# Performance work log

Hardware: AMD Instinct MI355X
Metric: run time of the kernel (lower is better)

## Reference

```python
import jax, jax.numpy as jnp
import numpy as np

N = 100000      # nodes
E = 400000      # edges per relation
R = 4           # relations
D_IN, D_HID, D_OUT = 256, 256, 128


def setup_inputs() -> dict:
    key = jax.random.key(0)
    ks = jax.random.split(key, 6)
    x = jax.random.normal(ks[0], (N, D_IN), jnp.float32)
    src = jax.random.randint(ks[1], (R, E), 0, N)
    dst = jax.random.randint(ks[2], (R, E), 0, N)
    # glorot-ish init for per-relation GraphConv weights
    W1 = jax.random.normal(ks[3], (R, D_IN, D_HID), jnp.float32) * (1.0 / np.sqrt(D_IN))
    b1 = jnp.zeros((R, D_HID), jnp.float32)
    W2 = jax.random.normal(ks[4], (R, D_HID, D_OUT), jnp.float32) * (1.0 / np.sqrt(D_HID))
    b2 = jnp.zeros((R, D_OUT), jnp.float32)
    return {"x": x, "src": src, "dst": dst, "W1": W1, "b1": b1, "W2": W2, "b2": b2}


def _rel_graphconv(x, src, dst, W, b):
    """DGL GraphConv with norm='both': D_dst^{-1/2} A D_src^{-1/2} X W + b.
    x: [N, din]; src/dst: [E]; W: [din, dout]; b: [dout]."""
    n = x.shape[0]
    xw = x @ W                                                   # [N, dout]
    ones = jnp.ones(src.shape, jnp.float32)
    out_deg = jnp.maximum(jax.ops.segment_sum(ones, src, num_segments=n), 1.0)
    in_deg = jnp.maximum(jax.ops.segment_sum(ones, dst, num_segments=n), 1.0)
    msg = xw[src] * (out_deg[src] ** -0.5)[:, None]              # [E, dout] gather + src-norm
    agg = jax.ops.segment_sum(msg, dst, num_segments=n)          # [N, dout] scatter-add
    return agg * (in_deg ** -0.5)[:, None] + b


def _hetero_layer(x, src, dst, W, b):
    # HeteroGraphConv(aggregate='sum'): run GraphConv per relation, sum results.
    conv = jax.vmap(_rel_graphconv, in_axes=(None, 0, 0, 0, 0))
    return jnp.sum(conv(x, src, dst, W, b), axis=0)              # [N, dout]


def reference(x, src, dst, W1, b1, W2, b2):
    h = jax.nn.relu(_hetero_layer(x, src, dst, W1, b1))
    return _hetero_layer(h, src, dst, W2, b2)
```

## Files before the change

### kernel.cpp

```cpp
#include <hip/hip_runtime.h>


#define RELS 4
#define DIN 256
#define DHID 256
#define DOUT 128

typedef short short8 __attribute__((ext_vector_type(8)));
typedef unsigned short ushort8 __attribute__((ext_vector_type(8)));
typedef float f32x4 __attribute__((ext_vector_type(4)));


__device__ __forceinline__ unsigned short f2bf(float f) {
    unsigned int u = __float_as_uint(f);
    u += 0x7FFFu + ((u >> 16) & 1u);
    return (unsigned short)(u >> 16);
}
__device__ __forceinline__ float bf2f(unsigned short u) {
    return __uint_as_float(((unsigned int)u) << 16);
}


__global__ void hist_kernel(const int* __restrict__ src, const int* __restrict__ dst,
                            int* __restrict__ cnt_src, int* __restrict__ cnt_dst,
                            int* __restrict__ rank, int E, int N) {
    int i = blockIdx.x * blockDim.x + threadIdx.x;
    if (i >= RELS * E) return;
    int r = i / E;
    atomicAdd(cnt_src + (size_t)r * N + src[i], 1);
    int rk = atomicAdd(cnt_dst + (size_t)r * N + dst[i], 1);
    rank[i] = rk;
}

__global__ void scan_norm(const int* __restrict__ counts, int* __restrict__ out,
                          int* __restrict__ blk_sums, int n, int SB,
                          const int* __restrict__ cnt, float* __restrict__ nrm, long nnorm) {
    if ((int)blockIdx.x < SB) {
        __shared__ int sh[256];
        int i = blockIdx.x * 256 + threadIdx.x;
        int v = (i < n) ? counts[i] : 0;
        sh[threadIdx.x] = v;
        __syncthreads();
#pragma unroll
        for (int off = 1; off < 256; off <<= 1) {
            int t = (threadIdx.x >= off) ? sh[threadIdx.x - off] : 0;
            __syncthreads();
            sh[threadIdx.x] += t;
            __syncthreads();
        }
        if (i < n) out[i] = sh[threadIdx.x] - v;
        if (threadIdx.x == 255) blk_sums[blockIdx.x] = sh[255];
    } else {
        long i = (long)(blockIdx.x - SB) * 256 + threadIdx.x;
        if (i < nnorm) nrm[i] = rsqrtf(fmaxf((float)cnt[i], 1.0f));
    }
}

__global__ void scan_sums(int* __restrict__ bs, int nb) {
    __shared__ int sh[256];
    __shared__ int carry;
    if (threadIdx.x == 0) carry = 0;
    __syncthreads();
    for (int base = 0; base < nb; base += 256) {
        int i = base + threadIdx.x;
        int v = (i < nb) ? bs[i] : 0;
        sh[threadIdx.x] = v;
        __syncthreads();
#pragma unroll
        for (int off = 1; off < 256; off <<= 1) {
            int t = (threadIdx.x >= off) ? sh[threadIdx.x - off] : 0;
            __syncthreads();
            sh[threadIdx.x] += t;
            __syncthreads();
        }
        if (i < nb) bs[i] = sh[threadIdx.x] - v + carry;
        int tot = sh[255];
        __syncthreads();
        if (threadIdx.x == 255) carry += tot;
        __syncthreads();
    }
}

__global__ void scan_add(int* __restrict__ out, const int* __restrict__ blk_sums,
                         int n, int total) {
    int i = blockIdx.x * 256 + threadIdx.x;
    if (i < n) out[i] += blk_sums[blockIdx.x];
    if (i == n - 1) out[n] = total;
}

__global__ void fill_kernel(const int* __restrict__ src, const int* __restrict__ dst,
                            const float* __restrict__ nsrc, const int* __restrict__ row_ptr,
                            const int* __restrict__ rank, int2* __restrict__ e_pack,
                            int E, int N) {
    int i = blockIdx.x * blockDim.x + threadIdx.x;
    if (i >= RELS * E) return;
    int r = i / E;
    int s = src[i];
    int pos = row_ptr[(size_t)r * N + dst[i]] + rank[i];
    e_pack[pos] = make_int2(s, __float_as_int(nsrc[(size_t)r * N + s]));
}


__global__ void prep_fused(const float* __restrict__ x, const float* __restrict__ W1,
                           const float* __restrict__ W2, const float* __restrict__ b1,
                           const float* __restrict__ b2,
                           unsigned short* __restrict__ x_bf, unsigned short* __restrict__ w1t,
                           unsigned short* __restrict__ w2t,
                           float* __restrict__ b1s, float* __restrict__ b2s, long n8x) {
    const int T1 = RELS * DIN * DHID;
    const int T2 = RELS * DHID * DOUT;
    long i = blockIdx.x * (long)blockDim.x + threadIdx.x;
    if (i < n8x) {
        const float4* ip = (const float4*)(x + i * 8);
        float4 v0 = ip[0], v1 = ip[1];
        ushort4 o0 = make_ushort4(f2bf(v0.x), f2bf(v0.y), f2bf(v0.z), f2bf(v0.w));
        ushort4 o1 = make_ushort4(f2bf(v1.x), f2bf(v1.y), f2bf(v1.z), f2bf(v1.w));
        ushort4* op = (ushort4*)(x_bf + i * 8);
        op[0] = o0; op[1] = o1;
    } else if (i < n8x + T1) {
        int j = (int)(i - n8x);
        int r = j / (DIN * DHID);
        int rem = j - r * (DIN * DHID);
        int k = rem / DHID, n = rem - k * DHID;
        w1t[(size_t)n * (RELS * DIN) + r * DIN + k] = f2bf(W1[j]);
    } else if (i < n8x + T1 + T2) {
        int j = (int)(i - n8x - T1);
        int r = j / (DHID * DOUT);
        int rem = j - r * (DHID * DOUT);
        int k = rem / DOUT, n = rem - k * DOUT;
        w2t[((size_t)r * DOUT + n) * DHID + k] = f2bf(W2[j]);
    } else if (i < n8x + T1 + T2 + DHID + DOUT) {
        int c = (int)(i - n8x - T1 - T2);
        if (c < DHID) {
            b1s[c] = b1[c] + b1[DHID + c] + b1[2 * DHID + c] + b1[3 * DHID + c];
        } else {
            int cc = c - DHID;
            b2s[cc] = b2[cc] + b2[DOUT + cc] + b2[2 * DOUT + cc] + b2[3 * DOUT + cc];
        }
    }
}


__device__ __forceinline__ void gload_lds16(const void* g, void* l) {
    __builtin_amdgcn_global_load_lds(
        (const __attribute__((address_space(1))) void*)g,
        (__attribute__((address_space(3))) void*)l, 16, 0, 0);
}

template <int MODE>
__global__ __launch_bounds__(256) void gemm_bf16(
    const unsigned short* __restrict__ A, const unsigned short* __restrict__ Bt,
    unsigned short* __restrict__ C, int M, int Nout, int K,
    const float* __restrict__ scale_or_bias, int cols_per_rel, int Nnodes) {
    __shared__ unsigned short smA[128 * 32];
    __shared__ unsigned short smB[128 * 32];
    const int tid = threadIdx.x;
    const int lane = tid & 63;
    const int wid = tid >> 6;
    const int wr = wid >> 1, wc = wid & 1;
    const int brow = blockIdx.x * 128, bcol = blockIdx.y * 128;

    f32x4 acc[4][4] = {};

    const int s = lane >> 4;
    const int rl = lane & 15;

    for (int k0 = 0; k0 < K; k0 += 32) {
#pragma unroll
        for (int q = 0; q < 2; ++q) {
            int c = q * 256 + tid;
            int cl = c ^ ((c >> 3) & 3);
            int row = cl >> 2, slot = cl & 3;
            int ga = brow + row; ga = ga < M ? ga : M - 1;
            size_t ldsoff = (size_t)(q * 256 + (tid & ~63)) * 16;
            gload_lds16(A + (size_t)ga * K + k0 + slot * 8, (char*)smA + ldsoff);
            gload_lds16(Bt + (size_t)(bcol + row) * K + k0 + slot * 8, (char*)smB + ldsoff);
        }
        asm volatile("s_waitcnt vmcnt(0)" ::: "memory");
        __syncthreads();

        short8 a[4], b[4];
#pragma unroll
        for (int i = 0; i < 4; ++i) {
            int r = wr * 64 + i * 16 + rl;
            int ch = r * 4 + (s ^ ((r >> 1) & 3));
            a[i] = *(const short8*)((const char*)smA + ch * 16);
        }
#pragma unroll
        for (int j = 0; j < 4; ++j) {
            int r = wc * 64 + j * 16 + rl;
            int ch = r * 4 + (s ^ ((r >> 1) & 3));
            b[j] = *(const short8*)((const char*)smB + ch * 16);
        }
#pragma unroll
        for (int i = 0; i < 4; ++i)
#pragma unroll
            for (int j = 0; j < 4; ++j)
                acc[i][j] = __builtin_amdgcn_mfma_f32_16x16x32_bf16(a[i], b[j], acc[i][j], 0, 0, 0);
        __syncthreads();
    }

    const int rq = lane >> 4;
    if (MODE == 0) {
        const int relid = bcol / cols_per_rel;
        const float* nsr = scale_or_bias + (size_t)relid * Nnodes;
#pragma unroll
        for (int i = 0; i < 4; ++i) {
            int rbase = brow + wr * 64 + i * 16 + rq * 4;
            float sc[4];
#pragma unroll
            for (int t = 0; t < 4; ++t) {
                int row = rbase + t;
                sc[t] = (row < M) ? nsr[row] : 0.f;
            }
#pragma unroll
            for (int j = 0; j < 4; ++j) {
                int col = bcol + wc * 64 + j * 16 + rl;
#pragma unroll
                for (int t = 0; t < 4; ++t) {
                    int row = rbase + t;
                    if (row < M) C[(size_t)row * Nout + col] = f2bf(acc[i][j][t] * sc[t]);
                }
            }
        }
    } else {
#pragma unroll
        for (int i = 0; i < 4; ++i) {
            int rbase = brow + wr * 64 + i * 16 + rq * 4;
#pragma unroll
            for (int j = 0; j < 4; ++j) {
                int col = bcol + wc * 64 + j * 16 + rl;
                float bb = scale_or_bias[col];
#pragma unroll
                for (int t = 0; t < 4; ++t) {
                    int row = rbase + t;
                    if (row < M) C[(size_t)row * Nout + col] = f2bf(fmaxf(acc[i][j][t] + bb, 0.f));
                }
            }
        }
    }
}


__global__ void gather1_agg(const unsigned short* __restrict__ x_bf,
                            const int* __restrict__ rp, const int2* __restrict__ e_pack,
                            const float* __restrict__ ndst,
                            unsigned short* __restrict__ agg4, int N) {
    long w = (blockIdx.x * (long)blockDim.x + threadIdx.x) >> 6;
    int d = (int)(w >> 2);
    if (d >= N) return;
    int r = (int)(w & 3);
    int lane = threadIdx.x & 63;
    int h = lane >> 5, l = lane & 31;
    int beg = rp[(size_t)r * N + d], end = rp[(size_t)r * N + d + 1];
    float acc0[8] = {}, acc1[8] = {};
    int e = beg + h;
    for (; e + 2 < end; e += 4) {
        int2 p0 = e_pack[e];
        int2 p1 = e_pack[e + 2];
        ushort8 v0 = *(const ushort8*)(x_bf + (size_t)p0.x * DIN + l * 8);
        ushort8 v1 = *(const ushort8*)(x_bf + (size_t)p1.x * DIN + l * 8);
        float ns0 = __int_as_float(p0.y);
        float ns1 = __int_as_float(p1.y);
#pragma unroll
        for (int j = 0; j < 8; ++j) {
            acc0[j] += ns0 * bf2f(v0[j]);
            acc1[j] += ns1 * bf2f(v1[j]);
        }
    }
    if (e < end) {
        int2 p0 = e_pack[e];
        ushort8 v0 = *(const ushort8*)(x_bf + (size_t)p0.x * DIN + l * 8);
        float ns0 = __int_as_float(p0.y);
#pragma unroll
        for (int j = 0; j < 8; ++j) acc0[j] += ns0 * bf2f(v0[j]);
    }
    float nd = ndst[(size_t)r * N + d];
    ushort8 o;
#pragma unroll
    for (int j = 0; j < 8; ++j) {
        float v = acc0[j] + acc1[j];
        v += __shfl_xor(v, 32);
        o[j] = f2bf(nd * v);
    }
    if (h == 0)
        __builtin_nontemporal_store(o, (ushort8*)(agg4 + (size_t)d * (RELS * DIN) + r * DIN + l * 8));
}

__global__ void gather2_fused(const unsigned short* __restrict__ hw4,
                              const int* __restrict__ rp, const int2* __restrict__ e_pack,
                              const float* __restrict__ ndst, const float* __restrict__ b2s,
                              float* __restrict__ out, int N) {
    int wid = (int)((blockIdx.x * (long)blockDim.x + threadIdx.x) >> 6);
    if (wid >= N) return;
    int lane = threadIdx.x & 63;
    int h = lane >> 5, l = lane & 31;
    float oacc[4] = {};
#pragma unroll
    for (int r = 0; r < RELS; ++r) {
        int beg = rp[(size_t)r * N + wid], end = rp[(size_t)r * N + wid + 1];
        float acc0[4] = {}, acc1[4] = {};
        int e = beg + h;
        for (; e + 2 < end; e += 4) {
            int s0 = e_pack[e].x;
            int s1 = e_pack[e + 2].x;
            ushort4 v0 = *(const ushort4*)(hw4 + (size_t)s0 * (RELS * DOUT) + r * DOUT + l * 4);
            ushort4 v1 = *(const ushort4*)(hw4 + (size_t)s1 * (RELS * DOUT) + r * DOUT + l * 4);
            acc0[0] += bf2f(v0.x); acc0[1] += bf2f(v0.y); acc0[2] += bf2f(v0.z); acc0[3] += bf2f(v0.w);
            acc1[0] += bf2f(v1.x); acc1[1] += bf2f(v1.y); acc1[2] += bf2f(v1.z); acc1[3] += bf2f(v1.w);
        }
        if (e < end) {
            int s0 = e_pack[e].x;
            ushort4 v0 = *(const ushort4*)(hw4 + (size_t)s0 * (RELS * DOUT) + r * DOUT + l * 4);
            acc0[0] += bf2f(v0.x); acc0[1] += bf2f(v0.y); acc0[2] += bf2f(v0.z); acc0[3] += bf2f(v0.w);
        }
        float nd = ndst[(size_t)r * N + wid];
#pragma unroll
        for (int j = 0; j < 4; ++j) oacc[j] += nd * (acc0[j] + acc1[j]);
    }
#pragma unroll
    for (int j = 0; j < 4; ++j) oacc[j] += __shfl_xor(oacc[j], 32);
    if (h == 0) {
        f32x4 o;
        o[0] = oacc[0] + b2s[l * 4 + 0];
        o[1] = oacc[1] + b2s[l * 4 + 1];
        o[2] = oacc[2] + b2s[l * 4 + 2];
        o[3] = oacc[3] + b2s[l * 4 + 3];
        __builtin_nontemporal_store(o, (f32x4*)(out + (size_t)wid * DOUT + l * 4));
    }
}


extern "C" void kernel_launch(void* const* d_in, const int* in_sizes, int n_in,
                              void* d_out, int out_size, void* d_ws, size_t ws_size,
                              hipStream_t stream) {
    const float* x   = (const float*)d_in[0];
    const int*   src = (const int*)d_in[1];
    const int*   dst = (const int*)d_in[2];
    const float* W1  = (const float*)d_in[3];
    const float* b1  = (const float*)d_in[4];
    const float* W2  = (const float*)d_in[5];
    const float* b2  = (const float*)d_in[6];
    float* out = (float*)d_out;

    const int N = in_sizes[0] / DIN;
    const int E = in_sizes[1] / RELS;
    const int RN = RELS * N;

    char* p = (char*)d_ws;
    int*   cnt_src = (int*)p;    p += (size_t)RN * sizeof(int);
    int*   cnt_dst = (int*)p;    p += (size_t)RN * sizeof(int);
    float* nsrc    = (float*)p;  p += (size_t)RN * sizeof(float);
    float* ndst    = (float*)p;  p += (size_t)RN * sizeof(float);
    int*   row_ptr = (int*)p;    p += ((size_t)RN + 16) * sizeof(int);
    int*   rank    = (int*)p;    p += (size_t)RELS * E * sizeof(int);
    int2*  e_pack  = (int2*)p;   p += (size_t)RELS * E * sizeof(int2);
    int*   blk_sums= (int*)p;    p += 2048 * sizeof(int);
    float* b1s     = (float*)p;  p += DHID * sizeof(float);
    float* b2s     = (float*)p;  p += DOUT * sizeof(float);
    unsigned short* x_bf = (unsigned short*)p; p += (size_t)N * DIN * sizeof(short);
    unsigned short* w1t  = (unsigned short*)p; p += (size_t)RELS * DIN * DHID * sizeof(short);
    unsigned short* w2t  = (unsigned short*)p; p += (size_t)RELS * DHID * DOUT * sizeof(short);
    unsigned short* h_bf = (unsigned short*)p; p += (size_t)N * DHID * sizeof(short);
    unsigned short* agg4 = (unsigned short*)p; p += (size_t)N * RELS * DIN * sizeof(short);
    unsigned short* hw4  = agg4;

    const long n8x = (long)N * DIN / 8;
    {
        long tot = n8x + RELS * DIN * DHID + RELS * DHID * DOUT + DHID + DOUT;
        prep_fused<<<(int)((tot + 255) / 256), 256, 0, stream>>>(
            x, W1, W2, b1, b2, x_bf, w1t, w2t, b1s, b2s, n8x);
    }

    hipMemsetAsync(cnt_src, 0, (size_t)2 * RN * sizeof(int), stream);
    {
        int total = RELS * E;
        hist_kernel<<<(total + 255) / 256, 256, 0, stream>>>(
            src, dst, cnt_src, cnt_dst, rank, E, N);
    }

    const int nscan = (RN + 255) / 256;
    {
        long nnorm = (long)2 * RN;
        int NB = (int)((nnorm + 255) / 256);
        scan_norm<<<nscan + NB, 256, 0, stream>>>(
            cnt_dst, row_ptr, blk_sums, RN, nscan, cnt_src, nsrc, nnorm);
    }
    scan_sums<<<1, 256, 0, stream>>>(blk_sums, nscan);
    scan_add<<<nscan, 256, 0, stream>>>(row_ptr, blk_sums, RN, RELS * E);

    {
        int total = RELS * E;
        fill_kernel<<<(total + 255) / 256, 256, 0, stream>>>(
            src, dst, nsrc, row_ptr, rank, e_pack, E, N);
    }

    const int gx = (N + 127) / 128;

    {
        long waves = (long)RELS * N;
        int blocks = (int)((waves + 3) / 4);
        gather1_agg<<<blocks, 256, 0, stream>>>(x_bf, row_ptr, e_pack, ndst, agg4, N);
        dim3 grid(gx, DHID / 128);
        gemm_bf16<1><<<grid, 256, 0, stream>>>(agg4, w1t, h_bf, N, DHID, RELS * DIN, b1s, 0, N);
    }

    {
        dim3 grid(gx, (RELS * DOUT) / 128);
        gemm_bf16<0><<<grid, 256, 0, stream>>>(h_bf, w2t, hw4, N, RELS * DOUT, DHID, nsrc, DOUT, N);
        int gblocks = (N + 3) / 4;
        gather2_fused<<<gblocks, 256, 0, stream>>>(hw4, row_ptr, e_pack, ndst, b2s, out, N);
    }
}
```

Before: 738.3 us.

## Fuse layer-1 neighbor aggregation with the relation GEMM in one kernel

Replaces the separate gather1_agg kernel and the MODE 1 GEMM with one fused1 kernel. Each 512-thread block aggregates 128 destination rows per relation into LDS, then runs MFMA against that relation's weight slice, accumulating over all four relations before applying bias and ReLU. This removes the write and re-read of the N x 1024 bf16 agg4 intermediate in global memory. In exchange, B operands are loaded straight from global without LDS staging, there is one block per 128 rows (about 782 blocks), and the gather and GEMM phases are serialized by barriers, so occupancy and latency hiding drop.

```diff
diff --git a/kernel.cpp b/kernel.cpp
--- a/kernel.cpp
+++ b/kernel.cpp
@@ -141,17 +141,121 @@
 }
 
 
+#define LDP 264
+
+__global__ __launch_bounds__(512) void fused1(
+    const unsigned short* __restrict__ x_bf, const int* __restrict__ rp,
+    const int2* __restrict__ e_pack, const float* __restrict__ ndst,
+    const unsigned short* __restrict__ w1t, const float* __restrict__ b1s,
+    unsigned short* __restrict__ h_bf, int N) {
+    __shared__ __align__(16) unsigned short smA[128 * LDP];
+    const int tid = threadIdx.x;
+    const int lane = tid & 63;
+    const int wid = tid >> 6;
+    const int wr = wid >> 2, wc = wid & 3;
+    const int brow = blockIdx.x * 128;
+    const int s = lane >> 4, rl = lane & 15;
+    const int h = lane >> 5, l = lane & 31;
+
+    f32x4 acc[4][4] = {};
+
+    for (int r = 0; r < RELS; ++r) {
+#pragma unroll 2
+        for (int t = 0; t < 16; ++t) {
+            int row = wid * 16 + t;
+            int node = brow + row;
+            int beg = 0, end = 0;
+            float nd = 0.f;
+            if (node < N) {
+                int base = r * N + node;
+                beg = rp[base]; end = rp[base + 1];
+                nd = ndst[base];
+            }
+            float acc0[8] = {}, acc1[8] = {};
+            int e = beg + h;
+            for (; e + 2 < end; e += 4) {
+                int2 p0 = e_pack[e];
+                int2 p1 = e_pack[e + 2];
+                ushort8 v0 = *(const ushort8*)(x_bf + (size_t)p0.x * DIN + l * 8);
+                ushort8 v1 = *(const ushort8*)(x_bf + (size_t)p1.x * DIN + l * 8);
+                float ns0 = __int_as_float(p0.y);
+                float ns1 = __int_as_float(p1.y);
+#pragma unroll
+                for (int j = 0; j < 8; ++j) {
+                    acc0[j] += ns0 * bf2f(v0[j]);
+                    acc1[j] += ns1 * bf2f(v1[j]);
+                }
+            }
+            if (e < end) {
+                int2 p0 = e_pack[e];
+                ushort8 v0 = *(const ushort8*)(x_bf + (size_t)p0.x * DIN + l * 8);
+                float ns0 = __int_as_float(p0.y);
+#pragma unroll
+                for (int j = 0; j < 8; ++j) acc0[j] += ns0 * bf2f(v0[j]);
+            }
+            ushort8 o;
+#pragma unroll
+            for (int j = 0; j < 8; ++j) {
+                float v = acc0[j] + acc1[j];
+                v += __shfl_xor(v, 32);
+                o[j] = f2bf(nd * v);
+            }
+            if (h == 0)
+                *(ushort8*)(smA + (size_t)row * LDP + l * 8) = o;
+        }
+        __syncthreads();
+
+        const unsigned short* wb = w1t + (size_t)r * DIN;
+#pragma unroll 2
+        for (int k0 = 0; k0 < 256; k0 += 32) {
+            short8 a[4], b[4];
+#pragma unroll
+            for (int i = 0; i < 4; ++i) {
+                int arow = wr * 64 + i * 16 + rl;
+                a[i] = *(const short8*)(smA + (size_t)arow * LDP + k0 + s * 8);
+            }
+#pragma unroll
+            for (int j = 0; j < 4; ++j) {
+                int col = wc * 64 + j * 16 + rl;
+                b[j] = *(const short8*)(wb + (size_t)col * (RELS * DIN) + k0 + s * 8);
+            }
+#pragma unroll
+            for (int i = 0; i < 4; ++i)
+#pragma unroll
+                for (int j = 0; j < 4; ++j)
+                    acc[i][j] = __builtin_amdgcn_mfma_f32_16x16x32_bf16(a[i], b[j], acc[i][j], 0, 0, 0);
+        }
+        __syncthreads();
+    }
+
+    const int rq = lane >> 4;
+#pragma unroll
+    for (int i = 0; i < 4; ++i) {
+        int rbase = brow + wr * 64 + i * 16 + rq * 4;
+#pragma unroll
+        for (int j = 0; j < 4; ++j) {
+            int col = wc * 64 + j * 16 + rl;
+            float bb = b1s[col];
+#pragma unroll
+            for (int t = 0; t < 4; ++t) {
+                int row = rbase + t;
+                if (row < N) h_bf[(size_t)row * DHID + col] = f2bf(fmaxf(acc[i][j][t] + bb, 0.f));
+            }
+        }
+    }
+}
+
+
 __device__ __forceinline__ void gload_lds16(const void* g, void* l) {
     __builtin_amdgcn_global_load_lds(
         (const __attribute__((address_space(1))) void*)g,
         (__attribute__((address_space(3))) void*)l, 16, 0, 0);
 }
 
-template <int MODE>
 __global__ __launch_bounds__(256) void gemm_bf16(
     const unsigned short* __restrict__ A, const unsigned short* __restrict__ Bt,
     unsigned short* __restrict__ C, int M, int Nout, int K,
-    const float* __restrict__ scale_or_bias, int cols_per_rel, int Nnodes) {
+    const float* __restrict__ nsrc_all, int cols_per_rel, int Nnodes) {
     __shared__ unsigned short smA[128 * 32];
     __shared__ unsigned short smB[128 * 32];
     const int tid = threadIdx.x;
@@ -201,91 +305,29 @@
     }
 
     const int rq = lane >> 4;
-    if (MODE == 0) {
-        const int relid = bcol / cols_per_rel;
-        const float* nsr = scale_or_bias + (size_t)relid * Nnodes;
-#pragma unroll
-        for (int i = 0; i < 4; ++i) {
-            int rbase = brow + wr * 64 + i * 16 + rq * 4;
-            float sc[4];
+    const int relid = bcol / cols_per_rel;
+    const float* nsr = nsrc_all + (size_t)relid * Nnodes;
+#pragma unroll
+    for (int i = 0; i < 4; ++i) {
+        int rbase = brow + wr * 64 + i * 16 + rq * 4;
+        float sc[4];
+#pragma unroll
+        for (int t = 0; t < 4; ++t) {
+            int row = rbase + t;
+            sc[t] = (row < M) ? nsr[row] : 0.f;
+        }
+#pragma unroll
+        for (int j = 0; j < 4; ++j) {
+            int col = bcol + wc * 64 + j * 16 + rl;
 #pragma unroll
             for (int t = 0; t < 4; ++t) {
                 int row = rbase + t;
-                sc[t] = (row < M) ? nsr[row] : 0.f;
-            }
-#pragma unroll
-            for (int j = 0; j < 4; ++j) {
-                int col = bcol + wc * 64 + j * 16 + rl;
-#pragma unroll
-                for (int t = 0; t < 4; ++t) {
-                    int row = rbase + t;
-                    if (row < M) C[(size_t)row * Nout + col] = f2bf(acc[i][j][t] * sc[t]);
-                }
-            }
-        }
-    } else {
-#pragma unroll
-        for (int i = 0; i < 4; ++i) {
-            int rbase = brow + wr * 64 + i * 16 + rq * 4;
-#pragma unroll
-            for (int j = 0; j < 4; ++j) {
-                int col = bcol + wc * 64 + j * 16 + rl;
-                float bb = scale_or_bias[col];
-#pragma unroll
-                for (int t = 0; t < 4; ++t) {
-                    int row = rbase + t;
-                    if (row < M) C[(size_t)row * Nout + col] = f2bf(fmaxf(acc[i][j][t] + bb, 0.f));
-                }
-            }
-        }
-    }
-}
-
-
-__global__ void gather1_agg(const unsigned short* __restrict__ x_bf,
-                            const int* __restrict__ rp, const int2* __restrict__ e_pack,
-                            const float* __restrict__ ndst,
-                            unsigned short* __restrict__ agg4, int N) {
-    long w = (blockIdx.x * (long)blockDim.x + threadIdx.x) >> 6;
-    int d = (int)(w >> 2);
-    if (d >= N) return;
-    int r = (int)(w & 3);
-    int lane = threadIdx.x & 63;
-    int h = lane >> 5, l = lane & 31;
-    int beg = rp[(size_t)r * N + d], end = rp[(size_t)r * N + d + 1];
-    float acc0[8] = {}, acc1[8] = {};
-    int e = beg + h;
-    for (; e + 2 < end; e += 4) {
-        int2 p0 = e_pack[e];
-        int2 p1 = e_pack[e + 2];
-        ushort8 v0 = *(const ushort8*)(x_bf + (size_t)p0.x * DIN + l * 8);
-        ushort8 v1 = *(const ushort8*)(x_bf + (size_t)p1.x * DIN + l * 8);
-        float ns0 = __int_as_float(p0.y);
-        float ns1 = __int_as_float(p1.y);
-#pragma unroll
-        for (int j = 0; j < 8; ++j) {
-            acc0[j] += ns0 * bf2f(v0[j]);
-            acc1[j] += ns1 * bf2f(v1[j]);
-        }
-    }
-    if (e < end) {
-        int2 p0 = e_pack[e];
-        ushort8 v0 = *(const ushort8*)(x_bf + (size_t)p0.x * DIN + l * 8);
-        float ns0 = __int_as_float(p0.y);
-#pragma unroll
-        for (int j = 0; j < 8; ++j) acc0[j] += ns0 * bf2f(v0[j]);
-    }
-    float nd = ndst[(size_t)r * N + d];
-    ushort8 o;
-#pragma unroll
-    for (int j = 0; j < 8; ++j) {
-        float v = acc0[j] + acc1[j];
-        v += __shfl_xor(v, 32);
-        o[j] = f2bf(nd * v);
-    }
-    if (h == 0)
-        __builtin_nontemporal_store(o, (ushort8*)(agg4 + (size_t)d * (RELS * DIN) + r * DIN + l * 8));
-}
+                if (row < M) C[(size_t)row * Nout + col] = f2bf(acc[i][j][t] * sc[t]);
+            }
+        }
+    }
+}
+
 
 __global__ void gather2_fused(const unsigned short* __restrict__ hw4,
                               const int* __restrict__ rp, const int2* __restrict__ e_pack,
@@ -362,8 +404,7 @@
     unsigned short* w1t  = (unsigned short*)p; p += (size_t)RELS * DIN * DHID * sizeof(short);
     unsigned short* w2t  = (unsigned short*)p; p += (size_t)RELS * DHID * DOUT * sizeof(short);
     unsigned short* h_bf = (unsigned short*)p; p += (size_t)N * DHID * sizeof(short);
-    unsigned short* agg4 = (unsigned short*)p; p += (size_t)N * RELS * DIN * sizeof(short);
-    unsigned short* hw4  = agg4;
+    unsigned short* hw4  = (unsigned short*)p; p += (size_t)N * RELS * DOUT * sizeof(short);
 
     const long n8x = (long)N * DIN / 8;
     {
@@ -397,17 +438,11 @@
 
     const int gx = (N + 127) / 128;
 
-    {
-        long waves = (long)RELS * N;
-        int blocks = (int)((waves + 3) / 4);
-        gather1_agg<<<blocks, 256, 0, stream>>>(x_bf, row_ptr, e_pack, ndst, agg4, N);
-        dim3 grid(gx, DHID / 128);
-        gemm_bf16<1><<<grid, 256, 0, stream>>>(agg4, w1t, h_bf, N, DHID, RELS * DIN, b1s, 0, N);
-    }
+    fused1<<<gx, 512, 0, stream>>>(x_bf, row_ptr, e_pack, ndst, w1t, b1s, h_bf, N);
 
     {
         dim3 grid(gx, (RELS * DOUT) / 128);
-        gemm_bf16<0><<<grid, 256, 0, stream>>>(h_bf, w2t, hw4, N, RELS * DOUT, DHID, nsrc, DOUT, N);
+        gemm_bf16<<<grid, 256, 0, stream>>>(h_bf, w2t, hw4, N, RELS * DOUT, DHID, nsrc, DOUT, N);
         int gblocks = (N + 3) / 4;
         gather2_fused<<<gblocks, 256, 0, stream>>>(hw4, row_ptr, e_pack, ndst, b2s, out, N);
     }
```

Measured after the change: 777.8 us. 1.05x slower.
